# Kernel optimization log

Measured on AMD Instinct MI355X. Metric: run time of the kernel, lower is better.

Reference implementation:

```python
import jax, jax.numpy as jnp
import numpy as np

G_MIN = 0.01

def _st(x):
    # straight-through: fwd zeroes |x|<G_MIN, bwd is identity
    hard = jnp.where(jnp.abs(x) < G_MIN, 0.0, x)
    return x + jax.lax.stop_gradient(hard - x)

def _inv(x):
    return 0.104 - 0.899 * jnp.tanh((x + 0.056) * 3.858)

def _activate(z):
    return 0.134 + 0.962 * jnp.tanh((z - 0.183) * 24.1)

def setup_inputs() -> dict:
    key = jax.random.key(0)
    k1, k2, k3 = jax.random.split(key, 3)
    M, n_in, n_out = 8192, 4096, 4096
    a_previous = jax.random.uniform(k1, (M, n_in), dtype=jnp.float32)
    theta = jax.random.uniform(k2, (n_out, n_in + 2), dtype=jnp.float32)
    # mimic __init__ scaling of last two columns
    theta = theta.at[:, -1].multiply(100.0)
    theta = theta.at[:, -2].set(0.1788 / (1 - 0.1788) * (jnp.sum(jnp.abs(theta[:, :-3]), axis=1) + jnp.abs(theta[:, -1])))
    aging_decay = jax.random.uniform(k3, (n_out, n_in + 2), minval=0.9, maxval=1.0, dtype=jnp.float32)
    return {"a_previous": a_previous, "theta": theta, "aging_decay": aging_decay}

def reference(a_previous, theta, aging_decay):
    M = a_previous.shape[0]
    # aged + straight-through theta
    th = _st(theta * aging_decay)                     # [m, n]
    g = jnp.abs(th)
    W = g / jnp.sum(g, axis=1, keepdims=True)         # [m, n]
    # augment input with ones and zeros columns
    a_aug = jnp.concatenate([a_previous,
                             jnp.ones((M, 1), a_previous.dtype),
                             jnp.zeros((M, 1), a_previous.dtype)], axis=1)  # [M, n]
    inv_a = _inv(a_aug)
    pt = (th >= 0).astype(W.dtype)
    nt = (th < 0).astype(W.dtype)
    # z[j,i] = sum_k a_aug[j,k]*W[i,k]*pt[i,k] + inv_a[j,k]*W[i,k]*nt[i,k]
    z = a_aug @ (W * pt).T + inv_a @ (W * nt).T       # [M, m]
    return _activate(z)
```

## Files before the change

### kernel.cpp

```cpp
#include <hip/hip_runtime.h>
#include <hip/hip_bf16.h>
#include <stdint.h>

#define M_DIM 8192
#define N_DIM 4096
#define K_IN  4096
#define NC    (K_IN + 2)
#define K_DIM (2 * K_IN)

#define BM 256
#define BN 256
#define BKB 128
#define NT (K_DIM / BKB)

typedef __attribute__((ext_vector_type(4))) int i32x4;
typedef __attribute__((ext_vector_type(16))) int i32x16;

__device__ __forceinline__ float fast_tanh(float y) {
  float e = __expf(2.0f * y);
  return 1.0f - 2.0f * __builtin_amdgcn_rcpf(1.0f + e);
}

__device__ __forceinline__ int q8(float x) {
  return (int)__builtin_rintf(x);
}

__global__ __launch_bounds__(256) void prep_A(const float* __restrict__ a,
                                              int8_t* __restrict__ Ap) {
  int idx = blockIdx.x * 256 + threadIdx.x;
  int j  = idx >> 10;
  int k4 = (idx & 1023) << 2;
  float4 v = reinterpret_cast<const float4*>(a)[idx];
  float xs[4] = {v.x, v.y, v.z, v.w};
  int lw = 0, rw = 0;
#pragma unroll
  for (int t = 0; t < 4; ++t) {
    float x = xs[t];
    int ql = q8(x * 127.0f);
    float inv = 0.104f - 0.899f * fast_tanh((x + 0.056f) * 3.858f);
    int qr = q8(inv * 127.0f);
    lw |= (ql & 255) << (8 * t);
    rw |= (qr & 255) << (8 * t);
  }
  size_t base = (size_t)j * K_DIM + k4;
  *reinterpret_cast<int*>(Ap + base)        = lw;
  *reinterpret_cast<int*>(Ap + base + K_IN) = rw;
}

__global__ __launch_bounds__(256) void prep_B(const float* __restrict__ theta,
                                              const float* __restrict__ aging,
                                              int8_t* __restrict__ Bp,
                                              float* __restrict__ corr,
                                              float* __restrict__ sc) {
  __shared__ float th_s[NC];
  __shared__ float red_s[256];
  __shared__ float red_m[256];
  int i = blockIdx.x;
  int tid = threadIdx.x;
  const float* tr = theta + (size_t)i * NC;
  const float* ar = aging + (size_t)i * NC;
  float psum = 0.f, pmax = 0.f;
  for (int k = tid; k < NC; k += 256) {
    float th = tr[k] * ar[k];
    if (fabsf(th) < 0.01f) th = 0.f;
    th_s[k] = th;
    psum += fabsf(th);
    if (k < K_IN) pmax = fmaxf(pmax, fabsf(th));
  }
  red_s[tid] = psum;
  red_m[tid] = pmax;
  __syncthreads();
  for (int s = 128; s > 0; s >>= 1) {
    if (tid < s) {
      red_s[tid] += red_s[tid + s];
      red_m[tid] = fmaxf(red_m[tid], red_m[tid + s]);
    }
    __syncthreads();
  }
  float inv_sum = 1.0f / red_s[0];
  float maxabs  = red_m[0];
  float qs = 127.0f / maxabs;
  int8_t* out = Bp + (size_t)i * K_DIM;
  for (int k0 = tid * 4; k0 < K_IN; k0 += 1024) {
    int pw = 0, nw = 0;
#pragma unroll
    for (int t = 0; t < 4; ++t) {
      float th = th_s[k0 + t];
      int q = q8(fabsf(th) * qs);
      if (th >= 0.f) pw |= (q & 255) << (8 * t);
      else           nw |= (q & 255) << (8 * t);
    }
    *reinterpret_cast<int*>(out + k0)         = pw;
    *reinterpret_cast<int*>(out + K_IN + k0)  = nw;
  }
  if (tid == 0) {
    float th1 = th_s[K_IN];
    float th2 = th_s[K_IN + 1];
    float w1 = fabsf(th1) * inv_sum;
    float w2 = fabsf(th2) * inv_sum;
    float inv1 = 0.104f - 0.899f * fast_tanh((1.0f + 0.056f) * 3.858f);
    float inv0 = 0.104f - 0.899f * fast_tanh((0.0f + 0.056f) * 3.858f);
    float c = (th1 >= 0.f) ? w1 : w1 * inv1;
    c += (th2 >= 0.f) ? 0.0f : w2 * inv0;
    corr[i] = c;
    sc[i] = maxabs * inv_sum * (1.0f / 16129.0f);
  }
}

__global__ __launch_bounds__(512, 2) void gemm_fused(const int8_t* __restrict__ A,
                                                     const int8_t* __restrict__ B,
                                                     const float* __restrict__ corr,
                                                     const float* __restrict__ sc,
                                                     float* __restrict__ C) {
  extern __shared__ char lds[];
  const int tid  = threadIdx.x;
  const int lane = tid & 63;
  const int wid  = tid >> 6;
  const int wr   = wid >> 2;
  const int wc   = wid & 3;
  const int fr   = lane & 31;
  const int kg   = lane >> 5;

  const int bid = (int)blockIdx.x;
  const int sw  = (bid & 7) * 64 + (bid >> 3);
  const int bm0 = (sw >> 4) * BM;
  const int bn0 = (sw & 15) * BN;

  const int colsw = (((tid & 7) ^ ((tid >> 3) & 7) ^ ((tid >> 6) & 3)) << 4);
  const int8_t* gA = A + (size_t)(bm0 + (tid >> 3)) * K_DIM + colsw;
  const int8_t* gB = B + (size_t)(bn0 + (tid >> 3)) * K_DIM + colsw;
  const int dst_t = tid * 16;

  const int flip = (((fr & 7) ^ ((fr >> 3) & 3)) << 4);
  int csk[4];
#pragma unroll
  for (int ks = 0; ks < 4; ++ks) csk[ks] = (ks * 32 + kg * 16) ^ flip;
  const int aRow = (wr * 128 + fr) * BKB;
  const int bRow = (wc * 64 + fr) * BKB;

  i32x16 acc[4][2] = {};

#define STAGE(ISA, H, T) do {                                                        \
    const int8_t* _g = (ISA) ? gA : gB;                                              \
    const size_t _go = (size_t)((H) * 128) * K_DIM + (size_t)(T) * BKB;              \
    char* _l = lds + (((T) & 1) * 65536) + ((ISA) ? 0 : 32768) + (H) * 16384 + dst_t; \
    __builtin_amdgcn_global_load_lds(                                                \
        (const __attribute__((address_space(1))) unsigned int*)(_g + _go),           \
        (__attribute__((address_space(3))) unsigned int*)_l, 16, 0, 0);              \
    __builtin_amdgcn_global_load_lds(                                                \
        (const __attribute__((address_space(1))) unsigned int*)(_g + _go + (size_t)64 * K_DIM), \
        (__attribute__((address_space(3))) unsigned int*)(_l + 8192), 16, 0, 0);     \
  } while (0)

#define MFMA32(a, b, c) __builtin_amdgcn_mfma_i32_32x32x32_i8((a), (b), (c), 0, 0, 0)

  STAGE(1, 0, 0); STAGE(1, 1, 0); STAGE(0, 0, 0); STAGE(0, 1, 0);
  STAGE(0, 0, 1); STAGE(0, 1, 1);
  asm volatile("s_waitcnt vmcnt(4)" ::: "memory");
  __builtin_amdgcn_s_barrier();

#pragma unroll 2
  for (int W = 0; W < NT; ++W) {
    const char* pa = lds + (W & 1) * 65536 + aRow;
    const char* pb = lds + (W & 1) * 65536 + 32768 + bRow;
    i32x4 af[2][4], bf[2][4];

#pragma unroll
    for (int ks = 0; ks < 4; ++ks) {
      af[0][ks] = *(const i32x4*)(pa + csk[ks]);
      bf[0][ks] = *(const i32x4*)(pb + csk[ks]);
      af[1][ks] = *(const i32x4*)(pa + 32 * BKB + csk[ks]);
      bf[1][ks] = *(const i32x4*)(pb + 32 * BKB + csk[ks]);
    }
    if (W + 1 < NT) { STAGE(1, 0, W + 1); STAGE(1, 1, W + 1); }
    __builtin_amdgcn_s_barrier();
    __builtin_amdgcn_s_setprio(1);
#pragma unroll
    for (int ks = 0; ks < 4; ++ks)
#pragma unroll
      for (int m = 0; m < 2; ++m)
#pragma unroll
        for (int n = 0; n < 2; ++n)
          acc[m][n] = MFMA32(af[m][ks], bf[n][ks], acc[m][n]);
    __builtin_amdgcn_s_setprio(0);

#pragma unroll
    for (int ks = 0; ks < 4; ++ks) {
      af[0][ks] = *(const i32x4*)(pa + 2 * 32 * BKB + csk[ks]);
      af[1][ks] = *(const i32x4*)(pa + 3 * 32 * BKB + csk[ks]);
    }
    if (W + 2 < NT) { STAGE(0, 0, W + 2); STAGE(0, 1, W + 2); }
    if (W < NT - 2) { asm volatile("s_waitcnt vmcnt(4)" ::: "memory"); }
    else            { asm volatile("s_waitcnt vmcnt(0)" ::: "memory"); }
    __builtin_amdgcn_s_barrier();
    __builtin_amdgcn_s_setprio(1);
#pragma unroll
    for (int ks = 0; ks < 4; ++ks)
#pragma unroll
      for (int m = 0; m < 2; ++m)
#pragma unroll
        for (int n = 0; n < 2; ++n)
          acc[m + 2][n] = MFMA32(af[m][ks], bf[n][ks], acc[m + 2][n]);
    __builtin_amdgcn_s_setprio(0);
  }

#pragma unroll
  for (int n = 0; n < 2; ++n) {
    const int col = bn0 + wc * 64 + n * 32 + fr;
    const float cr = corr[col];
    const float s  = sc[col];
#pragma unroll
    for (int mi = 0; mi < 4; ++mi) {
      const int rbase = bm0 + wr * 128 + mi * 32 + 4 * kg;
#pragma unroll
      for (int r = 0; r < 16; ++r) {
        const int row = rbase + (r & 3) + 8 * (r >> 2);
        float z = (float)acc[mi][n][r] * s + cr;
        float e = __expf((z - 0.183f) * 48.2f);
        C[(size_t)row * N_DIM + col] = 1.096f - 1.924f * __builtin_amdgcn_rcpf(1.0f + e);
      }
    }
  }
#undef STAGE
#undef MFMA32
}

extern "C" void kernel_launch(void* const* d_in, const int* in_sizes, int n_in,
                              void* d_out, int out_size, void* d_ws, size_t ws_size,
                              hipStream_t stream) {
  (void)in_sizes; (void)n_in; (void)out_size; (void)ws_size;
  const float* a_prev = (const float*)d_in[0];
  const float* theta  = (const float*)d_in[1];
  const float* aging  = (const float*)d_in[2];
  float* out = (float*)d_out;

  char* ws = (char*)d_ws;
  int8_t* Ap = (int8_t*)ws;
  int8_t* Bp = (int8_t*)(ws + (size_t)M_DIM * K_DIM);
  float* corr = (float*)(ws + (size_t)M_DIM * K_DIM + (size_t)N_DIM * K_DIM);
  float* sc   = corr + N_DIM;

  prep_A<<<(M_DIM * K_IN / 4) / 256, 256, 0, stream>>>(a_prev, Ap);
  prep_B<<<N_DIM, 256, 0, stream>>>(theta, aging, Bp, corr, sc);

  (void)hipFuncSetAttribute((const void*)gemm_fused,
                            hipFuncAttributeMaxDynamicSharedMemorySize, 131072);
  gemm_fused<<<dim3((M_DIM / BM) * (N_DIM / BN)), dim3(512), 131072, stream>>>(Ap, Bp, corr, sc, out);
}
```

Baseline: 304.5 us.

## Pre-pack B in MFMA fragment layout and load it directly into registers

prep_B now writes the int8 weight matrix in a fragment-major layout matching the MFMA operand order for each 32-column block and K-slice. The GEMM then skips staging B through LDS and has each wave load its B fragments straight from global memory into registers. Only A goes through LDS, which halves shared memory use to 64KB. The main loop is rescheduled so A fragments are read once per tile and B loads are prefetched one step ahead. In exchange, each wave issues its own global B loads, with more redundant L2 traffic across waves that share columns and greater exposure to global latency.

```diff
diff --git a/kernel.cpp b/kernel.cpp
--- a/kernel.cpp
+++ b/kernel.cpp
@@ -12,6 +12,7 @@
 #define BN 256
 #define BKB 128
 #define NT (K_DIM / BKB)
+#define NBLK (N_DIM / 32)
 
 typedef __attribute__((ext_vector_type(4))) int i32x4;
 typedef __attribute__((ext_vector_type(16))) int i32x16;
@@ -49,7 +50,7 @@
 
 __global__ __launch_bounds__(256) void prep_B(const float* __restrict__ theta,
                                               const float* __restrict__ aging,
-                                              int8_t* __restrict__ Bp,
+                                              int8_t* __restrict__ Bt,
                                               float* __restrict__ corr,
                                               float* __restrict__ sc) {
   __shared__ float th_s[NC];
@@ -80,7 +81,8 @@
   float inv_sum = 1.0f / red_s[0];
   float maxabs  = red_m[0];
   float qs = 127.0f / maxabs;
-  int8_t* out = Bp + (size_t)i * K_DIM;
+  const int nb = i >> 5;
+  const int li = i & 31;
   for (int k0 = tid * 4; k0 < K_IN; k0 += 1024) {
     int pw = 0, nw = 0;
 #pragma unroll
@@ -90,8 +92,13 @@
       if (th >= 0.f) pw |= (q & 255) << (8 * t);
       else           nw |= (q & 255) << (8 * t);
     }
-    *reinterpret_cast<int*>(out + k0)         = pw;
-    *reinterpret_cast<int*>(out + K_IN + k0)  = nw;
+    const int t8  = k0 >> 7;
+    const int ks  = (k0 >> 5) & 3;
+    const int kg  = (k0 >> 4) & 1;
+    const size_t byte_p = ((size_t)(t8 * 128 + nb) << 12) + (ks << 10)
+                        + ((kg * 32 + li) << 4) + (k0 & 15);
+    *reinterpret_cast<int*>(Bt + byte_p) = pw;
+    *reinterpret_cast<int*>(Bt + byte_p + ((size_t)4096 << 12)) = nw;
   }
   if (tid == 0) {
     float th1 = th_s[K_IN];
@@ -108,7 +115,7 @@
 }
 
 __global__ __launch_bounds__(512, 2) void gemm_fused(const int8_t* __restrict__ A,
-                                                     const int8_t* __restrict__ B,
+                                                     const int8_t* __restrict__ Bt,
                                                      const float* __restrict__ corr,
                                                      const float* __restrict__ sc,
                                                      float* __restrict__ C) {
@@ -128,7 +135,6 @@
 
   const int colsw = (((tid & 7) ^ ((tid >> 3) & 7) ^ ((tid >> 6) & 3)) << 4);
   const int8_t* gA = A + (size_t)(bm0 + (tid >> 3)) * K_DIM + colsw;
-  const int8_t* gB = B + (size_t)(bn0 + (tid >> 3)) * K_DIM + colsw;
   const int dst_t = tid * 16;
 
   const int flip = (((fr & 7) ^ ((fr >> 3) & 3)) << 4);
@@ -136,72 +142,78 @@
 #pragma unroll
   for (int ks = 0; ks < 4; ++ks) csk[ks] = (ks * 32 + kg * 16) ^ flip;
   const int aRow = (wr * 128 + fr) * BKB;
-  const int bRow = (wc * 64 + fr) * BKB;
+
+  const int nb0 = (bn0 >> 5) + wc * 2;
+  const int8_t* gBt = Bt + ((size_t)nb0 << 12) + lane * 16;
 
   i32x16 acc[4][2] = {};
-
-#define STAGE(ISA, H, T) do {                                                        \
-    const int8_t* _g = (ISA) ? gA : gB;                                              \
-    const size_t _go = (size_t)((H) * 128) * K_DIM + (size_t)(T) * BKB;              \
-    char* _l = lds + (((T) & 1) * 65536) + ((ISA) ? 0 : 32768) + (H) * 16384 + dst_t; \
-    __builtin_amdgcn_global_load_lds(                                                \
-        (const __attribute__((address_space(1))) unsigned int*)(_g + _go),           \
-        (__attribute__((address_space(3))) unsigned int*)_l, 16, 0, 0);              \
-    __builtin_amdgcn_global_load_lds(                                                \
-        (const __attribute__((address_space(1))) unsigned int*)(_g + _go + (size_t)64 * K_DIM), \
-        (__attribute__((address_space(3))) unsigned int*)(_l + 8192), 16, 0, 0);     \
+  i32x4 a[4][4];
+  i32x4 bn[2][4];
+
+#define STAGE_A(T) do {                                                              \
+    char* _lb = lds + ((T) & 1) * 32768;                                             \
+    const size_t _go = (size_t)(T) * BKB;                                            \
+    _Pragma("unroll")                                                                \
+    for (int _q = 0; _q < 4; ++_q)                                                   \
+      __builtin_amdgcn_global_load_lds(                                              \
+          (const __attribute__((address_space(1))) unsigned int*)(gA + _go + (size_t)_q * 64 * K_DIM), \
+          (__attribute__((address_space(3))) unsigned int*)(_lb + _q * 8192 + dst_t), 16, 0, 0); \
   } while (0)
 
-#define MFMA32(a, b, c) __builtin_amdgcn_mfma_i32_32x32x32_i8((a), (b), (c), 0, 0, 0)
-
-  STAGE(1, 0, 0); STAGE(1, 1, 0); STAGE(0, 0, 0); STAGE(0, 1, 0);
-  STAGE(0, 0, 1); STAGE(0, 1, 1);
-  asm volatile("s_waitcnt vmcnt(4)" ::: "memory");
+#define LOADB(dst, T, n) do {                                                        \
+    _Pragma("unroll")                                                                \
+    for (int _ks = 0; _ks < 4; ++_ks)                                                \
+      dst[_ks] = *(const i32x4*)(gBt + (((size_t)(T) * 128 + (n)) << 12) + (_ks << 10)); \
+  } while (0)
+
+#define READ_A(T) do {                                                               \
+    const char* _pa = lds + ((T) & 1) * 32768 + aRow;                                \
+    _Pragma("unroll")                                                                \
+    for (int _m = 0; _m < 4; ++_m)                                                   \
+      _Pragma("unroll")                                                              \
+      for (int _ks = 0; _ks < 4; ++_ks)                                              \
+        a[_m][_ks] = *(const i32x4*)(_pa + _m * 32 * BKB + csk[_ks]);                \
+  } while (0)
+
+#define MFMA32(x, y, c) __builtin_amdgcn_mfma_i32_32x32x32_i8((x), (y), (c), 0, 0, 0)
+
+  STAGE_A(0); STAGE_A(1);
+  LOADB(bn[0], 0, 0); LOADB(bn[1], 0, 1);
+  asm volatile("s_waitcnt vmcnt(0)" ::: "memory");
   __builtin_amdgcn_s_barrier();
+  asm volatile("" ::: "memory");
+  READ_A(0);
 
 #pragma unroll 2
   for (int W = 0; W < NT; ++W) {
-    const char* pa = lds + (W & 1) * 65536 + aRow;
-    const char* pb = lds + (W & 1) * 65536 + 32768 + bRow;
-    i32x4 af[2][4], bf[2][4];
-
-#pragma unroll
-    for (int ks = 0; ks < 4; ++ks) {
-      af[0][ks] = *(const i32x4*)(pa + csk[ks]);
-      bf[0][ks] = *(const i32x4*)(pb + csk[ks]);
-      af[1][ks] = *(const i32x4*)(pa + 32 * BKB + csk[ks]);
-      bf[1][ks] = *(const i32x4*)(pb + 32 * BKB + csk[ks]);
-    }
-    if (W + 1 < NT) { STAGE(1, 0, W + 1); STAGE(1, 1, W + 1); }
+    if (W < NT - 1) { asm volatile("s_waitcnt vmcnt(8)" ::: "memory"); }
+    else            { asm volatile("s_waitcnt vmcnt(4)" ::: "memory"); }
+    __builtin_amdgcn_s_setprio(1);
+#pragma unroll
+    for (int ks = 0; ks < 4; ++ks)
+#pragma unroll
+      for (int m = 0; m < 4; ++m)
+        acc[m][0] = MFMA32(a[m][ks], bn[0][ks], acc[m][0]);
+    __builtin_amdgcn_s_setprio(0);
+    __builtin_amdgcn_sched_barrier(0);
+    if (W + 1 < NT) LOADB(bn[0], W + 1, 0);
+
+    if (W < NT - 1) { asm volatile("s_waitcnt vmcnt(4)" ::: "memory"); }
+    else            { asm volatile("s_waitcnt vmcnt(0)" ::: "memory"); }
+    asm volatile("s_waitcnt lgkmcnt(0)" ::: "memory");
     __builtin_amdgcn_s_barrier();
+    asm volatile("" ::: "memory");
     __builtin_amdgcn_s_setprio(1);
 #pragma unroll
     for (int ks = 0; ks < 4; ++ks)
 #pragma unroll
-      for (int m = 0; m < 2; ++m)
-#pragma unroll
-        for (int n = 0; n < 2; ++n)
-          acc[m][n] = MFMA32(af[m][ks], bf[n][ks], acc[m][n]);
+      for (int m = 0; m < 4; ++m)
+        acc[m][1] = MFMA32(a[m][ks], bn[1][ks], acc[m][1]);
     __builtin_amdgcn_s_setprio(0);
-
-#pragma unroll
-    for (int ks = 0; ks < 4; ++ks) {
-      af[0][ks] = *(const i32x4*)(pa + 2 * 32 * BKB + csk[ks]);
-      af[1][ks] = *(const i32x4*)(pa + 3 * 32 * BKB + csk[ks]);
-    }
-    if (W + 2 < NT) { STAGE(0, 0, W + 2); STAGE(0, 1, W + 2); }
-    if (W < NT - 2) { asm volatile("s_waitcnt vmcnt(4)" ::: "memory"); }
-    else            { asm volatile("s_waitcnt vmcnt(0)" ::: "memory"); }
-    __builtin_amdgcn_s_barrier();
-    __builtin_amdgcn_s_setprio(1);
-#pragma unroll
-    for (int ks = 0; ks < 4; ++ks)
-#pragma unroll
-      for (int m = 0; m < 2; ++m)
-#pragma unroll
-        for (int n = 0; n < 2; ++n)
-          acc[m + 2][n] = MFMA32(af[m][ks], bf[n][ks], acc[m + 2][n]);
-    __builtin_amdgcn_s_setprio(0);
+    __builtin_amdgcn_sched_barrier(0);
+    if (W + 1 < NT) READ_A(W + 1);
+    if (W + 2 < NT) STAGE_A(W + 2);
+    if (W + 1 < NT) LOADB(bn[1], W + 1, 1);
   }
 
 #pragma unroll
@@ -221,7 +233,9 @@
       }
     }
   }
-#undef STAGE
+#undef STAGE_A
+#undef LOADB
+#undef READ_A
 #undef MFMA32
 }
 
@@ -236,14 +250,14 @@
 
   char* ws = (char*)d_ws;
   int8_t* Ap = (int8_t*)ws;
-  int8_t* Bp = (int8_t*)(ws + (size_t)M_DIM * K_DIM);
+  int8_t* Bt = (int8_t*)(ws + (size_t)M_DIM * K_DIM);
   float* corr = (float*)(ws + (size_t)M_DIM * K_DIM + (size_t)N_DIM * K_DIM);
   float* sc   = corr + N_DIM;
 
   prep_A<<<(M_DIM * K_IN / 4) / 256, 256, 0, stream>>>(a_prev, Ap);
-  prep_B<<<N_DIM, 256, 0, stream>>>(theta, aging, Bp, corr, sc);
+  prep_B<<<N_DIM, 256, 0, stream>>>(theta, aging, Bt, corr, sc);
 
   (void)hipFuncSetAttribute((const void*)gemm_fused,
-                            hipFuncAttributeMaxDynamicSharedMemorySize, 131072);
-  gemm_fused<<<dim3((M_DIM / BM) * (N_DIM / BN)), dim3(512), 131072, stream>>>(Ap, Bp, corr, sc, out);
-}
+                            hipFuncAttributeMaxDynamicSharedMemorySize, 65536);
+  gemm_fused<<<dim3((M_DIM / BM) * (N_DIM / BN)), dim3(512), 65536, stream>>>(Ap, Bt, corr, sc, out);
+}
```

New measurement: 386.8 us. 1.27x slower.
